# Optimization experiments

Hardware: AMD Instinct MI355X
Metric: run time of the kernel (lower is better)

## Reference

```python
import jax, jax.numpy as jnp
import numpy as np

D_MODEL = 1024
NUM_HEADS = 16
D_K = D_MODEL // NUM_HEADS          # 64
D_ROPE = int(D_K * 0.5)             # 32
ROPE_BASE = 10000.0


def _rope(x):
    # x: [L, B, H, D_K]; rotate first D_ROPE features, pass the rest through.
    L = x.shape[0]
    d = D_ROPE
    theta = 1.0 / (ROPE_BASE ** (jnp.arange(0, d, 2, dtype=jnp.float32) / d))  # [d/2]
    idx_theta = jnp.arange(L, dtype=jnp.float32)[:, None] * theta[None, :]     # [L, d/2]
    idx_theta2 = jnp.concatenate([idx_theta, idx_theta], axis=-1)              # [L, d]
    cos = jnp.cos(idx_theta2)[:, None, None, :].astype(x.dtype)
    sin = jnp.sin(idx_theta2)[:, None, None, :].astype(x.dtype)
    x_rope, x_pass = x[..., :d], x[..., d:]
    neg_half = jnp.concatenate([-x_rope[..., d // 2:], x_rope[..., :d // 2]], axis=-1)
    x_rope = x_rope * cos + neg_half * sin
    return jnp.concatenate([x_rope, x_pass], axis=-1)


def setup_inputs() -> dict:
    key = jax.random.key(0)
    k1, k2 = jax.random.split(key)
    L, B = 2048, 2
    x = jax.random.normal(k1, (L, B, D_MODEL), dtype=jnp.float32)
    # xavier_uniform-like init for in_proj_weight [3*d_model, d_model]
    limit = float(np.sqrt(6.0 / (3 * D_MODEL + D_MODEL)))
    in_proj_weight = jax.random.uniform(k2, (3 * D_MODEL, D_MODEL),
                                        minval=-limit, maxval=limit, dtype=jnp.float32)
    return {"x": x, "in_proj_weight": in_proj_weight}


def reference(x, in_proj_weight):
    L, B, _ = x.shape
    # fused QKV projection: [L, B, 3*d_model]
    qkv = jnp.einsum('ed,lbd->lbe', in_proj_weight, x)
    # NOTE: faithful to original quirk — reshape to per-head blocks of 3*d_k,
    # then chunk along last dim.
    qkv = qkv.reshape(L, B, NUM_HEADS, 3 * D_K)
    q, k, v = qkv[..., :D_K], qkv[..., D_K:2 * D_K], qkv[..., 2 * D_K:]
    q = _rope(q)
    k = _rope(k)
    # [L,B,H,dk] -> [H,B,L,dk]
    q, k, v = (jnp.swapaxes(t, 0, 2) for t in (q, k, v))
    scale = 1.0 / jnp.sqrt(jnp.asarray(D_K, dtype=x.dtype))
    scores = jnp.einsum('hbqd,hbkd->hbqk', q, k) * scale      # [H,B,L,L]
    attn = jax.nn.softmax(scores, axis=-1)
    out = jnp.einsum('hbqk,hbkd->hbqd', attn, v)              # [H,B,L,dk]
    out = jnp.transpose(out, (1, 2, 0, 3)).reshape(B, L, D_MODEL)
    return jnp.swapaxes(out, 0, 1)                            # [L,B,D] (batch_first falsy)
```

## Files before the change

kernel.cpp:

```cpp
#include <hip/hip_runtime.h>
#include <hip/hip_bf16.h>
#include <cstdint>
#include <cstddef>

#define L_SEQ 2048
#define BATCH 2
#define DM 1024
#define NH 16
#define DK 64
#define QKV_N 3072
#define HEAD_STRIDE 192
#define NX (4096 * 1024)
#define NW (3072 * 1024)

typedef short short8_t __attribute__((ext_vector_type(8)));
typedef short short4_t __attribute__((ext_vector_type(4)));
typedef float f32x4 __attribute__((ext_vector_type(4)));

#define MFMA32(a, b, c) __builtin_amdgcn_mfma_f32_16x16x32_bf16(a, b, c, 0, 0, 0)
#define MFMA16(a, b, c) __builtin_amdgcn_mfma_f32_16x16x16bf16_1k(a, b, c, 0, 0, 0)
#define EXP2(x) __builtin_amdgcn_exp2f(x)

static __device__ __forceinline__ unsigned pk2(float a, float b) {
  __hip_bfloat162 h = __float22bfloat162_rn(make_float2(a, b));
  union { __hip_bfloat162 h; unsigned u; } v;
  v.h = h;
  return v.u;
}

static __device__ __forceinline__ void async_copy16(const unsigned short* g,
                                                    unsigned short* l) {
  __builtin_amdgcn_global_load_lds(
      (const __attribute__((address_space(1))) unsigned int*)g,
      (__attribute__((address_space(3))) unsigned int*)l, 16, 0, 0);
}

__global__ __launch_bounds__(256) void cast_kernel(
    const float* __restrict__ X, const float* __restrict__ W,
    unsigned short* __restrict__ dst) {
  const int e = (blockIdx.x * 256 + threadIdx.x) * 8;
  const float* src = (e < NX) ? &X[e] : &W[e - NX];
  const float4 v0 = *(const float4*)src;
  const float4 v1 = *(const float4*)(src + 4);
  union { short8_t s8; unsigned u[4]; } o;
  o.u[0] = pk2(v0.x, v0.y);
  o.u[1] = pk2(v0.z, v0.w);
  o.u[2] = pk2(v1.x, v1.y);
  o.u[3] = pk2(v1.z, v1.w);
  *(short8_t*)&dst[e] = o.s8;
}

__global__ __launch_bounds__(256) void qkv_gemm_bf16(
    const unsigned short* __restrict__ Xb, const unsigned short* __restrict__ Wb,
    unsigned short* __restrict__ qkvb) {
  __shared__ __align__(16) unsigned short As[2][128 * 32];
  __shared__ __align__(16) unsigned short Bs[2][128 * 32];
  const int t = threadIdx.x;
  const int w = t >> 6;
  const int lane = t & 63;
  const int L16 = lane & 15;
  const int quad = lane >> 4;
  const int m0 = blockIdx.y * 128;
  const int n0 = blockIdx.x * 128;
  const int wm = w & 1;
  const int wn = w >> 1;

  const int c0 = w * 128 + lane;
  const int c1 = c0 + 64;
  const unsigned short* gA0 = Xb + (size_t)(m0 + (c0 >> 2)) * 1024 + (c0 & 3) * 8;
  const unsigned short* gA1 = Xb + (size_t)(m0 + (c1 >> 2)) * 1024 + (c1 & 3) * 8;
  const unsigned short* gB0 = Wb + (size_t)(n0 + (c0 >> 2)) * 1024 + (c0 & 3) * 8;
  const unsigned short* gB1 = Wb + (size_t)(n0 + (c1 >> 2)) * 1024 + (c1 & 3) * 8;

  f32x4 acc[4][4];
#pragma unroll
  for (int i = 0; i < 4; ++i)
#pragma unroll
    for (int j = 0; j < 4; ++j) acc[i][j] = (f32x4){0.f, 0.f, 0.f, 0.f};

  async_copy16(gA0, &As[0][w * 1024]);
  async_copy16(gA1, &As[0][w * 1024 + 512]);
  async_copy16(gB0, &Bs[0][w * 1024]);
  async_copy16(gB1, &Bs[0][w * 1024 + 512]);

#define GBODY(K0, BUF)                                                        \
  {                                                                           \
    __syncthreads();           \
    if ((K0) + 32 < 1024) {                                                   \
      async_copy16(gA0 + (K0) + 32, &As[(BUF) ^ 1][w * 1024]);                \
      async_copy16(gA1 + (K0) + 32, &As[(BUF) ^ 1][w * 1024 + 512]);          \
      async_copy16(gB0 + (K0) + 32, &Bs[(BUF) ^ 1][w * 1024]);                \
      async_copy16(gB1 + (K0) + 32, &Bs[(BUF) ^ 1][w * 1024 + 512]);          \
    }                                                                         \
    short8_t af[4], bfr[4];                                                   \
    _Pragma("unroll") for (int mt = 0; mt < 4; ++mt)                          \
        af[mt] = *(const short8_t*)                                           \
            &As[BUF][(wm * 64 + mt * 16 + L16) * 32 + quad * 8];              \
    _Pragma("unroll") for (int nt = 0; nt < 4; ++nt)                          \
        bfr[nt] = *(const short8_t*)                                          \
            &Bs[BUF][(wn * 64 + nt * 16 + L16) * 32 + quad * 8];              \
    _Pragma("unroll") for (int mt = 0; mt < 4; ++mt)                          \
        _Pragma("unroll") for (int nt = 0; nt < 4; ++nt)                      \
            acc[mt][nt] = MFMA32(af[mt], bfr[nt], acc[mt][nt]);               \
  }

  for (int k0 = 0; k0 < 1024; k0 += 64) {
    GBODY(k0, 0)
    GBODY(k0 + 32, 1)
  }

  const int nbase = n0 + wn * 64 + L16;
  const int chunk = (n0 >> 6) + wn;
  const int type = chunk % 3;
  if (type == 2) {
#pragma unroll
    for (int mt = 0; mt < 4; ++mt) {
      const int mbase = m0 + wm * 64 + mt * 16 + quad * 4;
#pragma unroll
      for (int reg = 0; reg < 4; ++reg) {
        const size_t r = (size_t)(mbase + reg) * QKV_N + nbase;
        const unsigned u0 = pk2(acc[mt][0][reg], acc[mt][1][reg]);
        const unsigned u1 = pk2(acc[mt][2][reg], acc[mt][3][reg]);
        qkvb[r]      = (unsigned short)u0;
        qkvb[r + 16] = (unsigned short)(u0 >> 16);
        qkvb[r + 32] = (unsigned short)u1;
        qkvb[r + 48] = (unsigned short)(u1 >> 16);
      }
    }
  } else {
    const float qs = (type == 0) ? 0.18033688011112042f : 1.0f;
    const float theta = exp2f(-(float)L16 * 0.8304820237218405f);
#pragma unroll
    for (int mt = 0; mt < 4; ++mt) {
      const int mbase = m0 + wm * 64 + mt * 16 + quad * 4;
      const int lb = mbase >> 1;
      float sv[2], cv[2];
      __sincosf((float)lb * theta, &sv[0], &cv[0]);
      __sincosf((float)(lb + 1) * theta, &sv[1], &cv[1]);
#pragma unroll
      for (int reg = 0; reg < 4; ++reg) {
        const int li = reg >> 1;
        const float v0 = acc[mt][0][reg], v1 = acc[mt][1][reg];
        const float r0 = v0 * cv[li] - v1 * sv[li];
        const float r1 = v1 * cv[li] + v0 * sv[li];
        const size_t r = (size_t)(mbase + reg) * QKV_N + nbase;
        const unsigned u0 = pk2(r0 * qs, r1 * qs);
        const unsigned u1 = pk2(acc[mt][2][reg] * qs, acc[mt][3][reg] * qs);
        qkvb[r]      = (unsigned short)u0;
        qkvb[r + 16] = (unsigned short)(u0 >> 16);
        qkvb[r + 32] = (unsigned short)u1;
        qkvb[r + 48] = (unsigned short)(u1 >> 16);
      }
    }
  }
}

__global__ __launch_bounds__(256, 2) void attn_mfma_kernel(
    const unsigned short* __restrict__ qkvb, float* __restrict__ out) {
  __shared__ __align__(16) unsigned short Ks[2][4096];
  __shared__ __align__(16) unsigned short Vt[2][64][72];

  const int t = threadIdx.x;
  const int w = t >> 6;
  const int lane = t & 63;
  const int L16 = lane & 15;
  const int quad = lane >> 4;
  const int l0 = blockIdx.x * 128;
  const int b = blockIdx.y & 1;
  const int h = blockIdx.y >> 1;
  const int hoff = h * HEAD_STRIDE;

  const f32x4 z4 = {0.f, 0.f, 0.f, 0.f};

  short8_t bq[2][2];
#pragma unroll
  for (int mt = 0; mt < 2; ++mt)
#pragma unroll
    for (int kc = 0; kc < 2; ++kc)
      bq[mt][kc] = *(const short8_t*)
          &qkvb[((size_t)((l0 + w * 32 + mt * 16 + L16) * 2 + b)) * QKV_N +
                hoff + kc * 32 + quad * 8];

  f32x4 oc[2][4];
  float l_part[2] = {0.f, 0.f};
#pragma unroll
  for (int mt = 0; mt < 2; ++mt)
#pragma unroll
    for (int dt = 0; dt < 4; ++dt) oc[mt][dt] = z4;

  const int kr0 = w * 8 + (lane >> 3);
  const int kcs = ((lane & 7) ^ (lane >> 3)) * 8;
  const unsigned short* gK0 =
      qkvb + (size_t)(kr0 * 2 + b) * QKV_N + hoff + 64 + kcs;
  const unsigned short* gK1 = gK0 + (size_t)64 * QKV_N;
  const size_t kstep = (size_t)128 * QKV_N;

  const int vr4 = (t >> 4) * 4;
  const int vc4 = (t & 15) * 4;
  const int cgbase = vr4 >> 3;
  const int joff = vr4 & 7;
  short4_t rv[4];

#define LOAD_V(KT)                                                            \
  {                                                                           \
    const int j0 = (KT) * 64;                                                 \
    _Pragma("unroll") for (int r = 0; r < 4; ++r)                             \
        rv[r] = *(const short4_t*)&qkvb[((size_t)((j0 + vr4 + r) * 2 + b)) *  \
                                        QKV_N + hoff + 128 + vc4];            \
  }

  LOAD_V(0)
  async_copy16(gK0, &Ks[0][w * 512]);
  async_copy16(gK1, &Ks[0][w * 512 + 2048]);

  const int rsw = (L16 & 7);

#define ABODY(KT, BUF)                                                        \
  {                                                                           \
    {                                       \
      short4_t s0 = {rv[0][0], rv[1][0], rv[2][0], rv[3][0]};                 \
      short4_t s1 = {rv[0][1], rv[1][1], rv[2][1], rv[3][1]};                 \
      short4_t s2 = {rv[0][2], rv[1][2], rv[2][2], rv[3][2]};                 \
      short4_t s3 = {rv[0][3], rv[1][3], rv[2][3], rv[3][3]};                 \
      const int cg0 = (cgbase + ((vc4 >> 2) & 7)) & 7;                        \
      *(short4_t*)&Vt[BUF][vc4 + 0][cg0 * 8 + joff] = s0;                     \
      *(short4_t*)&Vt[BUF][vc4 + 1][cg0 * 8 + joff] = s1;                     \
      *(short4_t*)&Vt[BUF][vc4 + 2][cg0 * 8 + joff] = s2;                     \
      *(short4_t*)&Vt[BUF][vc4 + 3][cg0 * 8 + joff] = s3;                     \
    }                                                                         \
    __syncthreads();                                                          \
    if ((KT) + 1 < 32) {                                                      \
      async_copy16(gK0 + (size_t)((KT) + 1) * kstep, &Ks[(BUF) ^ 1][w * 512]);\
      async_copy16(gK1 + (size_t)((KT) + 1) * kstep,                          \
                   &Ks[(BUF) ^ 1][w * 512 + 2048]);                           \
      LOAD_V((KT) + 1)                                                        \
    }                                                                         \
    __builtin_amdgcn_s_setprio(1);                                            \
    _Pragma("unroll") for (int nt = 0; nt < 4; ++nt) {                        \
      const short8_t ak0 = *(const short8_t*)                                 \
          &Ks[BUF][(nt * 16 + L16) * 64 + (quad ^ rsw) * 8];                  \
      const short8_t ak1 = *(const short8_t*)                                 \
          &Ks[BUF][(nt * 16 + L16) * 64 + ((quad + 4) ^ rsw) * 8];            \
      f32x4 t0 = MFMA32(ak0, bq[0][0], z4);                                   \
      const f32x4 s0v = MFMA32(ak1, bq[0][1], t0);                            \
      f32x4 t1 = MFMA32(ak0, bq[1][0], z4);                                   \
      const f32x4 s1v = MFMA32(ak1, bq[1][1], t1);                            \
      float p0 = EXP2(s0v[0]), p1 = EXP2(s0v[1]);                             \
      float p2 = EXP2(s0v[2]), p3 = EXP2(s0v[3]);                             \
      l_part[0] += (p0 + p1) + (p2 + p3);                                     \
      union { short4_t s4; unsigned u[2]; } pu0;                              \
      pu0.u[0] = pk2(p0, p1);                                                 \
      pu0.u[1] = pk2(p2, p3);                                                 \
      float q0 = EXP2(s1v[0]), q1 = EXP2(s1v[1]);                             \
      float q2 = EXP2(s1v[2]), q3 = EXP2(s1v[3]);                             \
      l_part[1] += (q0 + q1) + (q2 + q3);                                     \
      union { short4_t s4; unsigned u[2]; } pu1;                              \
      pu1.u[0] = pk2(q0, q1);                                                 \
      pu1.u[1] = pk2(q2, q3);                                                 \
      _Pragma("unroll") for (int dt = 0; dt < 4; ++dt) {                      \
        const int d = dt * 16 + L16;                                          \
        const int g = 2 * nt + (quad >> 1);                                   \
        const int cg = (g + ((d >> 2) & 7)) & 7;                              \
        const short4_t vf =                                                   \
            *(const short4_t*)&Vt[BUF][d][cg * 8 + (quad & 1) * 4];           \
        oc[0][dt] = MFMA16(vf, pu0.s4, oc[0][dt]);                            \
        oc[1][dt] = MFMA16(vf, pu1.s4, oc[1][dt]);                            \
      }                                                                       \
    }                                                                         \
    __builtin_amdgcn_s_setprio(0);                                            \
  }

  for (int kt = 0; kt < 32; kt += 2) {
    ABODY(kt, 0)
    ABODY(kt + 1, 1)
  }

#pragma unroll
  for (int mt = 0; mt < 2; ++mt) {
    float l = l_part[mt];
    l += __shfl_xor(l, 16);
    l += __shfl_xor(l, 32);
    const float inv = 1.f / l;
    const int qrow = l0 + w * 32 + mt * 16 + L16;
    const size_t rbase = ((size_t)(qrow * 2 + b)) * DM + h * DK;
#pragma unroll
    for (int dt = 0; dt < 4; ++dt) {
      *(float4*)&out[rbase + dt * 16 + quad * 4] =
          make_float4(oc[mt][dt][0] * inv, oc[mt][dt][1] * inv,
                      oc[mt][dt][2] * inv, oc[mt][dt][3] * inv);
    }
  }
}

extern "C" void kernel_launch(void* const* d_in, const int* in_sizes, int n_in,
                              void* d_out, int out_size, void* d_ws,
                              size_t ws_size, hipStream_t stream) {
  const float* x = (const float*)d_in[0];
  const float* w = (const float*)d_in[1];
  float* out = (float*)d_out;
  unsigned short* bf = (unsigned short*)d_ws;
  unsigned short* Xb = bf;
  unsigned short* Wb = bf + NX;
  unsigned short* qkvb =
      (unsigned short*)((char*)d_ws + (16u << 20));

  cast_kernel<<<(NX + NW) / (256 * 8), 256, 0, stream>>>(x, w, bf);
  qkv_gemm_bf16<<<dim3(QKV_N / 128, (L_SEQ * BATCH) / 128), 256, 0, stream>>>(
      Xb, Wb, qkvb);
  attn_mfma_kernel<<<dim3(L_SEQ / 128, NH * BATCH), 256, 0, stream>>>(qkvb, out);
}
```

Measured before the change: 164.4 us.

## Write V pre-transposed from GEMM epilogue and async-copy it in attention

The QKV GEMM epilogue now writes Q/K into a compact [M,2048] buffer and writes V transposed per (batch,head) as [d][L], so the attention kernel can stream V tiles with async global-to-LDS copies and an XOR swizzle, the same way it loads K. This removes the register-staged V load, the in-kernel transpose and its LDS scatter writes from the attention loop. In exchange, the epilogue does strided 4-byte V stores (one per two rows), which may be less coalesced, and it uses an extra workspace region.

```diff
diff --git a/kernel.cpp b/kernel.cpp
--- a/kernel.cpp
+++ b/kernel.cpp
@@ -9,7 +9,7 @@
 #define NH 16
 #define DK 64
 #define QKV_N 3072
-#define HEAD_STRIDE 192
+#define QK_N 2048
 #define NX (4096 * 1024)
 #define NW (3072 * 1024)
 
@@ -52,7 +52,7 @@
 
 __global__ __launch_bounds__(256) void qkv_gemm_bf16(
     const unsigned short* __restrict__ Xb, const unsigned short* __restrict__ Wb,
-    unsigned short* __restrict__ qkvb) {
+    unsigned short* __restrict__ qkb, unsigned short* __restrict__ vtb) {
   __shared__ __align__(16) unsigned short As[2][128 * 32];
   __shared__ __align__(16) unsigned short Bs[2][128 * 32];
   const int t = threadIdx.x;
@@ -109,26 +109,26 @@
     GBODY(k0 + 32, 1)
   }
 
-  const int nbase = n0 + wn * 64 + L16;
   const int chunk = (n0 >> 6) + wn;
+  const int h = chunk / 3;
   const int type = chunk % 3;
   if (type == 2) {
 #pragma unroll
     for (int mt = 0; mt < 4; ++mt) {
       const int mbase = m0 + wm * 64 + mt * 16 + quad * 4;
-#pragma unroll
-      for (int reg = 0; reg < 4; ++reg) {
-        const size_t r = (size_t)(mbase + reg) * QKV_N + nbase;
-        const unsigned u0 = pk2(acc[mt][0][reg], acc[mt][1][reg]);
-        const unsigned u1 = pk2(acc[mt][2][reg], acc[mt][3][reg]);
-        qkvb[r]      = (unsigned short)u0;
-        qkvb[r + 16] = (unsigned short)(u0 >> 16);
-        qkvb[r + 32] = (unsigned short)u1;
-        qkvb[r + 48] = (unsigned short)(u1 >> 16);
+      const int lb = mbase >> 1;
+#pragma unroll
+      for (int nt = 0; nt < 4; ++nt) {
+        const int d = L16 + nt * 16;
+        const size_t r0 = ((size_t)(h * 64 + d)) * 2048 + lb;
+        const size_t r1 = ((size_t)((16 + h) * 64 + d)) * 2048 + lb;
+        *(unsigned*)&vtb[r0] = pk2(acc[mt][nt][0], acc[mt][nt][2]);
+        *(unsigned*)&vtb[r1] = pk2(acc[mt][nt][1], acc[mt][nt][3]);
       }
     }
   } else {
     const float qs = (type == 0) ? 0.18033688011112042f : 1.0f;
+    const int cbase = h * 128 + type * 64 + L16;
     const float theta = exp2f(-(float)L16 * 0.8304820237218405f);
 #pragma unroll
     for (int mt = 0; mt < 4; ++mt) {
@@ -143,22 +143,23 @@
         const float v0 = acc[mt][0][reg], v1 = acc[mt][1][reg];
         const float r0 = v0 * cv[li] - v1 * sv[li];
         const float r1 = v1 * cv[li] + v0 * sv[li];
-        const size_t r = (size_t)(mbase + reg) * QKV_N + nbase;
+        const size_t r = (size_t)(mbase + reg) * QK_N + cbase;
         const unsigned u0 = pk2(r0 * qs, r1 * qs);
         const unsigned u1 = pk2(acc[mt][2][reg] * qs, acc[mt][3][reg] * qs);
-        qkvb[r]      = (unsigned short)u0;
-        qkvb[r + 16] = (unsigned short)(u0 >> 16);
-        qkvb[r + 32] = (unsigned short)u1;
-        qkvb[r + 48] = (unsigned short)(u1 >> 16);
+        qkb[r]      = (unsigned short)u0;
+        qkb[r + 16] = (unsigned short)(u0 >> 16);
+        qkb[r + 32] = (unsigned short)u1;
+        qkb[r + 48] = (unsigned short)(u1 >> 16);
       }
     }
   }
 }
 
 __global__ __launch_bounds__(256, 2) void attn_mfma_kernel(
-    const unsigned short* __restrict__ qkvb, float* __restrict__ out) {
+    const unsigned short* __restrict__ qkb,
+    const unsigned short* __restrict__ vtb, float* __restrict__ out) {
   __shared__ __align__(16) unsigned short Ks[2][4096];
-  __shared__ __align__(16) unsigned short Vt[2][64][72];
+  __shared__ __align__(16) unsigned short Vs[2][4096];
 
   const int t = threadIdx.x;
   const int w = t >> 6;
@@ -168,7 +169,7 @@
   const int l0 = blockIdx.x * 128;
   const int b = blockIdx.y & 1;
   const int h = blockIdx.y >> 1;
-  const int hoff = h * HEAD_STRIDE;
+  const int vh = b * 16 + h;
 
   const f32x4 z4 = {0.f, 0.f, 0.f, 0.f};
 
@@ -178,8 +179,8 @@
 #pragma unroll
     for (int kc = 0; kc < 2; ++kc)
       bq[mt][kc] = *(const short8_t*)
-          &qkvb[((size_t)((l0 + w * 32 + mt * 16 + L16) * 2 + b)) * QKV_N +
-                hoff + kc * 32 + quad * 8];
+          &qkb[((size_t)((l0 + w * 32 + mt * 16 + L16) * 2 + b)) * QK_N +
+               h * 128 + kc * 32 + quad * 8];
 
   f32x4 oc[2][4];
   float l_part[2] = {0.f, 0.f};
@@ -191,49 +192,32 @@
   const int kr0 = w * 8 + (lane >> 3);
   const int kcs = ((lane & 7) ^ (lane >> 3)) * 8;
   const unsigned short* gK0 =
-      qkvb + (size_t)(kr0 * 2 + b) * QKV_N + hoff + 64 + kcs;
-  const unsigned short* gK1 = gK0 + (size_t)64 * QKV_N;
-  const size_t kstep = (size_t)128 * QKV_N;
-
-  const int vr4 = (t >> 4) * 4;
-  const int vc4 = (t & 15) * 4;
-  const int cgbase = vr4 >> 3;
-  const int joff = vr4 & 7;
-  short4_t rv[4];
-
-#define LOAD_V(KT)                                                            \
-  {                                                                           \
-    const int j0 = (KT) * 64;                                                 \
-    _Pragma("unroll") for (int r = 0; r < 4; ++r)                             \
-        rv[r] = *(const short4_t*)&qkvb[((size_t)((j0 + vr4 + r) * 2 + b)) *  \
-                                        QKV_N + hoff + 128 + vc4];            \
-  }
-
-  LOAD_V(0)
+      qkb + (size_t)(kr0 * 2 + b) * QK_N + h * 128 + 64 + kcs;
+  const unsigned short* gK1 = gK0 + (size_t)64 * QK_N;
+  const size_t kstep = (size_t)128 * QK_N;
+
+  const unsigned short* gV0 =
+      vtb + ((size_t)(vh * 64 + w * 8 + (lane >> 3))) * 2048 +
+      (((lane & 7) ^ (lane >> 3)) << 3);
+  const unsigned short* gV1 = gV0 + (size_t)32 * 2048;
+
   async_copy16(gK0, &Ks[0][w * 512]);
   async_copy16(gK1, &Ks[0][w * 512 + 2048]);
+  async_copy16(gV0, &Vs[0][w * 512]);
+  async_copy16(gV1, &Vs[0][w * 512 + 2048]);
 
   const int rsw = (L16 & 7);
+  const int vswz = (L16 & 7) << 3;
 
 #define ABODY(KT, BUF)                                                        \
   {                                                                           \
-    {                                       \
-      short4_t s0 = {rv[0][0], rv[1][0], rv[2][0], rv[3][0]};                 \
-      short4_t s1 = {rv[0][1], rv[1][1], rv[2][1], rv[3][1]};                 \
-      short4_t s2 = {rv[0][2], rv[1][2], rv[2][2], rv[3][2]};                 \
-      short4_t s3 = {rv[0][3], rv[1][3], rv[2][3], rv[3][3]};                 \
-      const int cg0 = (cgbase + ((vc4 >> 2) & 7)) & 7;                        \
-      *(short4_t*)&Vt[BUF][vc4 + 0][cg0 * 8 + joff] = s0;                     \
-      *(short4_t*)&Vt[BUF][vc4 + 1][cg0 * 8 + joff] = s1;                     \
-      *(short4_t*)&Vt[BUF][vc4 + 2][cg0 * 8 + joff] = s2;                     \
-      *(short4_t*)&Vt[BUF][vc4 + 3][cg0 * 8 + joff] = s3;                     \
-    }                                                                         \
-    __syncthreads();                                                          \
+    __syncthreads();        \
     if ((KT) + 1 < 32) {                                                      \
       async_copy16(gK0 + (size_t)((KT) + 1) * kstep, &Ks[(BUF) ^ 1][w * 512]);\
       async_copy16(gK1 + (size_t)((KT) + 1) * kstep,                          \
                    &Ks[(BUF) ^ 1][w * 512 + 2048]);                           \
-      LOAD_V((KT) + 1)                                                        \
+      async_copy16(gV0 + ((KT) + 1) * 64, &Vs[(BUF) ^ 1][w * 512]);           \
+      async_copy16(gV1 + ((KT) + 1) * 64, &Vs[(BUF) ^ 1][w * 512 + 2048]);    \
     }                                                                         \
     __builtin_amdgcn_s_setprio(1);                                            \
     _Pragma("unroll") for (int nt = 0; nt < 4; ++nt) {                        \
@@ -258,11 +242,8 @@
       pu1.u[0] = pk2(q0, q1);                                                 \
       pu1.u[1] = pk2(q2, q3);                                                 \
       _Pragma("unroll") for (int dt = 0; dt < 4; ++dt) {                      \
-        const int d = dt * 16 + L16;                                          \
-        const int g = 2 * nt + (quad >> 1);                                   \
-        const int cg = (g + ((d >> 2) & 7)) & 7;                              \
-        const short4_t vf =                                                   \
-            *(const short4_t*)&Vt[BUF][d][cg * 8 + (quad & 1) * 4];           \
+        const short4_t vf = *(const short4_t*)                                \
+            &Vs[BUF][(dt * 16 + L16) * 64 + ((nt * 16 + quad * 4) ^ vswz)];   \
         oc[0][dt] = MFMA16(vf, pu0.s4, oc[0][dt]);                            \
         oc[1][dt] = MFMA16(vf, pu1.s4, oc[1][dt]);                            \
       }                                                                       \
@@ -301,11 +282,14 @@
   unsigned short* bf = (unsigned short*)d_ws;
   unsigned short* Xb = bf;
   unsigned short* Wb = bf + NX;
-  unsigned short* qkvb =
+  unsigned short* qkb =
       (unsigned short*)((char*)d_ws + (16u << 20));
+  unsigned short* vtb =
+      (unsigned short*)((char*)d_ws + (32u << 20));
 
   cast_kernel<<<(NX + NW) / (256 * 8), 256, 0, stream>>>(x, w, bf);
   qkv_gemm_bf16<<<dim3(QKV_N / 128, (L_SEQ * BATCH) / 128), 256, 0, stream>>>(
-      Xb, Wb, qkvb);
-  attn_mfma_kernel<<<dim3(L_SEQ / 128, NH * BATCH), 256, 0, stream>>>(qkvb, out);
-}
+      Xb, Wb, qkb, vtb);
+  attn_mfma_kernel<<<dim3(L_SEQ / 128, NH * BATCH), 256, 0, stream>>>(qkb, vtb,
+                                                                      out);
+}
```

New measurement: 160.7 us. 2.3% less time.
